# Kernel tuning notes

Hardware: AMD Instinct MI355X
Metric: run time of the kernel (lower is better)

The kernel has to match this reference:

```python
import jax, jax.numpy as jnp
import numpy as np

EPS = 1e-5  # torch LayerNorm default
H = 8       # num_heads


def _ln(x, w, b):
    mu = jnp.mean(x, axis=-1, keepdims=True)
    var = jnp.mean(jnp.square(x - mu), axis=-1, keepdims=True)
    return (x - mu) * jax.lax.rsqrt(var + EPS) * w + b


def setup_inputs() -> dict:
    key = jax.random.key(0)
    ks = jax.random.split(key, 8)
    B, N, C = 4, 2048, 512
    d_ff = 4 * C
    g = lambda k, shape: jax.random.normal(k, shape, jnp.float32) * 0.02
    return {
        "x": jax.random.normal(ks[0], (B, N, C), jnp.float32),
        "e": jax.random.normal(ks[1], (B, N, C), jnp.float32),
        "w_qkv": g(ks[2], (C, 3 * C)),
        "w_s": g(ks[3], (C, C)),
        "w_gate": g(ks[4], (C, C)),
        "w_proj": g(ks[5], (C, C)),
        "b_proj": jnp.zeros((C,), jnp.float32),
        "ln1_w": jnp.ones((C,), jnp.float32), "ln1_b": jnp.zeros((C,), jnp.float32),
        "ln2_w": jnp.ones((C,), jnp.float32), "ln2_b": jnp.zeros((C,), jnp.float32),
        "ln3_w": jnp.ones((C,), jnp.float32), "ln3_b": jnp.zeros((C,), jnp.float32),
        "w_fc1": g(ks[6], (C, d_ff)), "b_fc1": jnp.zeros((d_ff,), jnp.float32),
        "w_fc2": g(ks[7], (d_ff, C)), "b_fc2": jnp.zeros((C,), jnp.float32),
    }


def reference(x, e, w_qkv, w_s, w_gate, w_proj, b_proj,
              ln1_w, ln1_b, ln2_w, ln2_b, ln3_w, ln3_b,
              w_fc1, b_fc1, w_fc2, b_fc2):
    B, N, C = x.shape
    D = C // H
    scale = D ** -0.5  # qk_scale=None -> (dim//num_heads)**-0.5

    # --- attention branch: x + attn(norm1(x), norm2(e)) ---
    xn = _ln(x, ln1_w, ln1_b)
    en = _ln(e, ln2_w, ln2_b)
    qkv = (xn @ w_qkv).reshape(B, N, 3, H, D).transpose(2, 0, 3, 1, 4)  # [3,B,H,N,D]
    q, k, v = qkv[0], qkv[1], qkv[2]
    s = (en @ w_s).reshape(B, N, H, D).transpose(0, 2, 1, 3)            # [B,H,N,D]
    attn = jax.nn.softmax(jnp.einsum('bhnd,bhmd->bhnm', q, k + s) * scale, axis=-1)
    o = jnp.einsum('bhnm,bhmd->bhnd', attn, v).transpose(0, 2, 1, 3).reshape(B, N, C)
    o = (o * (xn @ w_gate)) @ w_proj + b_proj
    x = x + o  # drop_path is identity (drop_prob=0)

    # --- MLP branch: x + mlp(norm3(x)) ---
    xn3 = _ln(x, ln3_w, ln3_b)
    h = jax.nn.gelu(xn3 @ w_fc1 + b_fc1, approximate=False)  # torch nn.GELU = exact erf
    return x + (h @ w_fc2 + b_fc2)
```

## Files before the change

kernel.cpp:

```cpp
#include <hip/hip_runtime.h>

typedef unsigned short u16;
typedef short s16;
typedef u16 u16x4 __attribute__((ext_vector_type(4)));
typedef u16 u16x8 __attribute__((ext_vector_type(8)));
typedef s16 s16x8 __attribute__((ext_vector_type(8)));
typedef float f32x4 __attribute__((ext_vector_type(4)));

__device__ __forceinline__ float b2f(u16 u) {
  union { unsigned int i; float f; } v;
  v.i = ((unsigned int)u) << 16;
  return v.f;
}
__device__ __forceinline__ u16 f2b(float f) {
  union { float f; unsigned int i; } v;
  v.f = f;
  unsigned int r = v.i + 0x7fffu + ((v.i >> 16) & 1u);
  return (u16)(r >> 16);
}

#define MFMA16(a, b, c) __builtin_amdgcn_mfma_f32_16x16x32_bf16(a, b, c, 0, 0, 0)

__device__ __forceinline__ void gld16(const u16* g, u16* l) {
  __builtin_amdgcn_global_load_lds(
      (const __attribute__((address_space(1))) void*)g,
      (__attribute__((address_space(3))) void*)l, 16, 0, 0);
}

__global__ __launch_bounds__(256) void ln12_kernel(
    const float* __restrict__ x, const float* __restrict__ e,
    const float* __restrict__ w1, const float* __restrict__ b1,
    const float* __restrict__ w2, const float* __restrict__ b2,
    u16* __restrict__ xn, u16* __restrict__ en) {
  int bid = blockIdx.x;
  const float *inv, *w, *bb;
  u16* out;
  if (bid < 2048) { inv = x; w = w1; bb = b1; out = xn; }
  else { bid -= 2048; inv = e; w = w2; bb = b2; out = en; }
  const int row = bid * 4 + (threadIdx.x >> 6);
  const int lane = threadIdx.x & 63;
  const float* p = inv + (size_t)row * 512 + lane * 8;
  f32x4 v0 = *(const f32x4*)p;
  f32x4 v1 = *(const f32x4*)(p + 4);
  float xv[8];
#pragma unroll
  for (int i = 0; i < 4; i++) { xv[i] = v0[i]; xv[4 + i] = v1[i]; }
  float s = 0.f;
#pragma unroll
  for (int i = 0; i < 8; i++) s += xv[i];
#pragma unroll
  for (int m = 1; m < 64; m <<= 1) s += __shfl_xor(s, m, 64);
  const float mu = s * (1.0f / 512.0f);
  float vs = 0.f;
#pragma unroll
  for (int i = 0; i < 8; i++) { const float d = xv[i] - mu; vs += d * d; }
#pragma unroll
  for (int m = 1; m < 64; m <<= 1) vs += __shfl_xor(vs, m, 64);
  const float r = rsqrtf(vs * (1.0f / 512.0f) + 1e-5f);
  const f32x4 w0 = *(const f32x4*)(w + lane * 8);
  const f32x4 w1v = *(const f32x4*)(w + lane * 8 + 4);
  const f32x4 bb0 = *(const f32x4*)(bb + lane * 8);
  const f32x4 bb1 = *(const f32x4*)(bb + lane * 8 + 4);
  u16x8 ov;
#pragma unroll
  for (int i = 0; i < 4; i++) {
    ov[i] = f2b((xv[i] - mu) * r * w0[i] + bb0[i]);
    ov[4 + i] = f2b((xv[4 + i] - mu) * r * w1v[i] + bb1[i]);
  }
  *(u16x8*)(out + (size_t)row * 512 + lane * 8) = ov;
}

__global__ __launch_bounds__(256) void ln_kernel(const float* __restrict__ inv,
                                                 const float* __restrict__ w,
                                                 const float* __restrict__ bvec,
                                                 u16* __restrict__ out) {
  const int row = blockIdx.x * 4 + (threadIdx.x >> 6);
  const int lane = threadIdx.x & 63;
  const float* p = inv + (size_t)row * 512 + lane * 8;
  f32x4 v0 = *(const f32x4*)p;
  f32x4 v1 = *(const f32x4*)(p + 4);
  float x[8];
#pragma unroll
  for (int i = 0; i < 4; i++) { x[i] = v0[i]; x[4 + i] = v1[i]; }
  float s = 0.f;
#pragma unroll
  for (int i = 0; i < 8; i++) s += x[i];
#pragma unroll
  for (int m = 1; m < 64; m <<= 1) s += __shfl_xor(s, m, 64);
  const float mu = s * (1.0f / 512.0f);
  float vs = 0.f;
#pragma unroll
  for (int i = 0; i < 8; i++) { const float d = x[i] - mu; vs += d * d; }
#pragma unroll
  for (int m = 1; m < 64; m <<= 1) vs += __shfl_xor(vs, m, 64);
  const float r = rsqrtf(vs * (1.0f / 512.0f) + 1e-5f);
  const f32x4 w0 = *(const f32x4*)(w + lane * 8);
  const f32x4 w1 = *(const f32x4*)(w + lane * 8 + 4);
  const f32x4 b0 = *(const f32x4*)(bvec + lane * 8);
  const f32x4 b1 = *(const f32x4*)(bvec + lane * 8 + 4);
  u16x8 ov;
#pragma unroll
  for (int i = 0; i < 4; i++) {
    ov[i] = f2b((x[i] - mu) * r * w0[i] + b0[i]);
    ov[4 + i] = f2b((x[4 + i] - mu) * r * w1[i] + b1[i]);
  }
  *(u16x8*)(out + (size_t)row * 512 + lane * 8) = ov;
}

__global__ __launch_bounds__(256) void wprep_kernel(
    const float* __restrict__ wq, const float* __restrict__ wsc,
    const float* __restrict__ wg, const float* __restrict__ wp,
    const float* __restrict__ w1, const float* __restrict__ w2,
    u16* __restrict__ wqgT, u16* __restrict__ wsT, u16* __restrict__ wpT,
    u16* __restrict__ wf1T, u16* __restrict__ wf2T) {
  __shared__ float T[64][65];
  int bid = blockIdx.x;
  const float* src; u16* dst; int K, N, ntiles;
  if (bid < 192)      { src = wq;  dst = wqgT;              K = 512;  N = 1536; ntiles = 24; }
  else if (bid < 256) { src = wg;  dst = wqgT + 1536 * 512; K = 512;  N = 512;  ntiles = 8; bid -= 192; }
  else if (bid < 320) { src = wsc; dst = wsT;               K = 512;  N = 512;  ntiles = 8; bid -= 256; }
  else if (bid < 384) { src = wp;  dst = wpT;               K = 512;  N = 512;  ntiles = 8; bid -= 320; }
  else if (bid < 640) { src = w1;  dst = wf1T;              K = 512;  N = 2048; ntiles = 32; bid -= 384; }
  else                { src = w2;  dst = wf2T;              K = 2048; N = 512;  ntiles = 8; bid -= 640; }
  const int n0 = (bid % ntiles) * 64, k0 = (bid / ntiles) * 64;
  const int c = threadIdx.x & 63, r0 = threadIdx.x >> 6;
#pragma unroll
  for (int i = 0; i < 16; i++) {
    const int r = i * 4 + r0;
    T[r][c] = src[(size_t)(k0 + r) * N + n0 + c];
  }
  __syncthreads();
#pragma unroll
  for (int i = 0; i < 16; i++) {
    const int r = i * 4 + r0;
    dst[(size_t)(n0 + r) * K + k0 + c] = f2b(T[c][r]);
  }
}

enum { EPI_NONE = 0, EPI_F32RES = 1, EPI_GELU = 2 };

template<int EPI, int BM>
__global__ __launch_bounds__(256) void mgemm(const u16* __restrict__ A,
                                             const u16* __restrict__ Bt,
                                             int M, int N, int K,
                                             u16* __restrict__ Cb, float* Cf,
                                             const float* __restrict__ bias,
                                             const float* resf) {
  constexpr int NT = (BM == 128) ? 4 : 2;
  constexpr int ACH = BM / 32;
  __shared__ u16 As[BM * 64];
  __shared__ u16 Bs[128 * 64];
  const int tid = threadIdx.x;
  const int wv = tid >> 6, lane = tid & 63;
  const int quad = lane >> 4, l16 = lane & 15;
  const int sw = l16 & 7;
  const int wrow = (BM == 128) ? (wv >> 1) * 64 : 0;
  const int wcol = (BM == 128) ? (wv & 1) * 64 : wv * 32;
  const int m0 = blockIdx.y * BM, n0 = blockIdx.x * 128;
  const int lrow = lane >> 3;
  const int lcs = ((lane & 7) ^ lrow) * 8;
  f32x4 acc[4][NT];
#pragma unroll
  for (int i = 0; i < 4; i++)
#pragma unroll
    for (int j = 0; j < NT; j++) acc[i][j] = (f32x4){0.f, 0.f, 0.f, 0.f};
  for (int k0 = 0; k0 < K; k0 += 64) {
    __syncthreads();
#pragma unroll
    for (int i = 0; i < ACH; i++) {
      const int ch = wv * ACH + i;
      gld16(A + (size_t)(m0 + ch * 8 + lrow) * K + k0 + lcs, &As[ch * 512]);
    }
#pragma unroll
    for (int i = 0; i < 4; i++) {
      const int ch = wv * 4 + i;
      gld16(Bt + (size_t)(n0 + ch * 8 + lrow) * K + k0 + lcs, &Bs[ch * 512]);
    }
    __syncthreads();
#pragma unroll
    for (int ks = 0; ks < 2; ks++) {
      s16x8 af[4], bf[NT];
#pragma unroll
      for (int mt = 0; mt < 4; mt++)
        af[mt] = *(const s16x8*)&As[(wrow + mt * 16 + l16) * 64 +
                                    (((ks * 4 + quad) ^ sw) * 8)];
#pragma unroll
      for (int nt = 0; nt < NT; nt++)
        bf[nt] = *(const s16x8*)&Bs[(wcol + nt * 16 + l16) * 64 +
                                    (((ks * 4 + quad) ^ sw) * 8)];
#pragma unroll
      for (int mt = 0; mt < 4; mt++)
#pragma unroll
        for (int nt = 0; nt < NT; nt++)
          acc[mt][nt] = MFMA16(af[mt], bf[nt], acc[mt][nt]);
    }
  }
#pragma unroll
  for (int nt = 0; nt < NT; nt++) {
    const int n = n0 + wcol + nt * 16 + l16;
    const float bn = (EPI != EPI_NONE) ? bias[n] : 0.f;
#pragma unroll
    for (int mt = 0; mt < 4; mt++) {
#pragma unroll
      for (int r = 0; r < 4; r++) {
        const int m = m0 + wrow + mt * 16 + quad * 4 + r;
        float v = acc[mt][nt][r] + bn;
        if (EPI == EPI_GELU)
          v = 0.5f * v * (1.0f + erff(v * 0.70710678118654752f));
        if (EPI == EPI_F32RES) {
          const size_t idx = (size_t)m * N + n;
          Cf[idx] = v + resf[idx];
        } else {
          Cb[(size_t)m * N + n] = f2b(v);
        }
      }
    }
  }
}

__global__ __launch_bounds__(256) void ksvt_kernel(const u16* __restrict__ qg,
                                                   const u16* __restrict__ sb,
                                                   u16* __restrict__ ksg,
                                                   u16* __restrict__ vtg) {
  __shared__ u16 T[64 * 72];
  const int bh = blockIdx.y;
  const int b = bh >> 3, h = bh & 7;
  const int kk0 = blockIdx.x * 64;
  const size_t rb = (size_t)b * 2048;
  const size_t base = (size_t)bh * 131072;
  const int row = threadIdx.x >> 2, cb = (threadIdx.x & 3) * 16;
  const u16* kp = qg + (rb + kk0 + row) * 2048 + 512 + h * 64 + cb;
  const u16* sp = sb + (rb + kk0 + row) * 512 + h * 64 + cb;
  const u16x8 k0v = *(const u16x8*)kp;
  const u16x8 k1v = *(const u16x8*)(kp + 8);
  const u16x8 s0v = *(const u16x8*)sp;
  const u16x8 s1v = *(const u16x8*)(sp + 8);
  u16x8 o0, o1;
#pragma unroll
  for (int i = 0; i < 8; i++) {
    o0[i] = f2b(b2f(k0v[i]) + b2f(s0v[i]));
    o1[i] = f2b(b2f(k1v[i]) + b2f(s1v[i]));
  }
  *(u16x8*)(ksg + base + (size_t)(kk0 + row) * 64 + cb) = o0;
  *(u16x8*)(ksg + base + (size_t)(kk0 + row) * 64 + cb + 8) = o1;
  const u16x8 v0v = *(const u16x8*)(kp + 512);
  const u16x8 v1v = *(const u16x8*)(kp + 520);
  *(u16x8*)&T[row * 72 + cb] = v0v;
  *(u16x8*)&T[row * 72 + cb + 8] = v1v;
  __syncthreads();
  u16x8 a0, a1;
#pragma unroll
  for (int i = 0; i < 8; i++) {
    a0[i] = T[(cb + i) * 72 + row];
    a1[i] = T[(cb + 8 + i) * 72 + row];
  }
  *(u16x8*)(vtg + base + (size_t)row * 2048 + kk0 + cb) = a0;
  *(u16x8*)(vtg + base + (size_t)row * 2048 + kk0 + cb + 8) = a1;
}

__global__ __launch_bounds__(256) void attn_kernel(const u16* __restrict__ qg,
                                                   const u16* __restrict__ ksg,
                                                   const u16* __restrict__ vtg,
                                                   u16* __restrict__ og) {
  __shared__ u16 KSs[64 * 64];
  __shared__ u16 VTs[64 * 64];
  __shared__ u16 PS[4][16 * 72];
  const int tid = threadIdx.x;
  const int w = tid >> 6, lane = tid & 63;
  const int quad = lane >> 4, l16 = lane & 15;
  const int sw = l16 & 7;
  const int q0 = blockIdx.x * 64;
  const int bh = blockIdx.y;
  const int h = bh & 7;
  const size_t rb = (size_t)(bh >> 3) * 2048;
  const size_t base = (size_t)bh * 131072;
  const int lrow = lane >> 3;
  const int lcs = ((lane & 7) ^ lrow) * 8;

  s16x8 aq[2];
  {
    const u16* qp = qg + (rb + q0 + w * 16 + l16) * 2048 + h * 64 + quad * 8;
#pragma unroll
    for (int ks = 0; ks < 2; ks++) {
      const u16x8 qv = *(const u16x8*)(qp + ks * 32);
      s16x8 t;
#pragma unroll
      for (int i = 0; i < 8; i++) t[i] = (s16)f2b(b2f(qv[i]) * 0.125f);
      aq[ks] = t;
    }
  }
  float m_run = -1e30f, l_run = 0.f;
  f32x4 oacc[4];
#pragma unroll
  for (int nt = 0; nt < 4; nt++) oacc[nt] = (f32x4){0.f, 0.f, 0.f, 0.f};

  for (int kt = 0; kt < 32; kt++) {
    const int kk0 = kt * 64;
    __syncthreads();
#pragma unroll
    for (int i = 0; i < 2; i++) {
      const int ch = w * 2 + i;
      gld16(ksg + base + (size_t)(kk0 + ch * 8 + lrow) * 64 + lcs, &KSs[ch * 512]);
      gld16(vtg + base + (size_t)(ch * 8 + lrow) * 2048 + kk0 + lcs, &VTs[ch * 512]);
    }
    __syncthreads();
    f32x4 sacc[4];
#pragma unroll
    for (int mt = 0; mt < 4; mt++) sacc[mt] = (f32x4){0.f, 0.f, 0.f, 0.f};
#pragma unroll
    for (int ks = 0; ks < 2; ks++) {
#pragma unroll
      for (int mt = 0; mt < 4; mt++) {
        const s16x8 kf = *(const s16x8*)&KSs[(mt * 16 + l16) * 64 +
                                             (((ks * 4 + quad) ^ sw) * 8)];
        sacc[mt] = MFMA16(kf, aq[ks], sacc[mt]);
      }
    }
    float lm = -1e30f;
#pragma unroll
    for (int mt = 0; mt < 4; mt++)
#pragma unroll
      for (int r = 0; r < 4; r++) lm = fmaxf(lm, sacc[mt][r]);
    lm = fmaxf(lm, __shfl_xor(lm, 16, 64));
    lm = fmaxf(lm, __shfl_xor(lm, 32, 64));
    const float mn = fmaxf(m_run, lm);
    const float alpha = __expf(m_run - mn);
    m_run = mn;
    float ls = 0.f;
#pragma unroll
    for (int mt = 0; mt < 4; mt++) {
#pragma unroll
      for (int r = 0; r < 4; r++) {
        const float pv = __expf(sacc[mt][r] - mn);
        sacc[mt][r] = pv;
        ls += pv;
      }
    }
    ls += __shfl_xor(ls, 16, 64);
    ls += __shfl_xor(ls, 32, 64);
    l_run = l_run * alpha + ls;
#pragma unroll
    for (int mt = 0; mt < 4; mt++) {
      u16x4 pk;
#pragma unroll
      for (int r = 0; r < 4; r++) pk[r] = f2b(sacc[mt][r]);
      *(u16x4*)&PS[w][l16 * 72 + mt * 16 + quad * 4] = pk;
    }
#pragma unroll
    for (int r = 0; r < 4; r++) {
      const float af = __shfl(alpha, quad * 4 + r, 64);
#pragma unroll
      for (int nt = 0; nt < 4; nt++) oacc[nt][r] *= af;
    }
#pragma unroll
    for (int ks = 0; ks < 2; ks++) {
      const s16x8 pf = *(const s16x8*)&PS[w][l16 * 72 + ks * 32 + quad * 8];
#pragma unroll
      for (int nt = 0; nt < 4; nt++) {
        const s16x8 vf = *(const s16x8*)&VTs[(nt * 16 + l16) * 64 +
                                             (((ks * 4 + quad) ^ sw) * 8)];
        oacc[nt] = MFMA16(pf, vf, oacc[nt]);
      }
    }
  }
#pragma unroll
  for (int r = 0; r < 4; r++) {
    const float linv = 1.0f / __shfl(l_run, quad * 4 + r, 64);
    const size_t grow = (rb + q0 + w * 16 + quad * 4 + r) * 2048 + 1536 + h * 64;
    const size_t rowb = (rb + q0 + w * 16 + quad * 4 + r) * 512 + h * 64;
#pragma unroll
    for (int nt = 0; nt < 4; nt++) {
      const float g = b2f(qg[grow + nt * 16 + l16]);
      og[rowb + nt * 16 + l16] = f2b(oacc[nt][r] * linv * g);
    }
  }
}

extern "C" void kernel_launch(void* const* d_in, const int* in_sizes, int n_in,
                              void* d_out, int out_size, void* d_ws, size_t ws_size,
                              hipStream_t stream) {
  const float* x      = (const float*)d_in[0];
  const float* e      = (const float*)d_in[1];
  const float* w_qkv  = (const float*)d_in[2];
  const float* w_s    = (const float*)d_in[3];
  const float* w_gate = (const float*)d_in[4];
  const float* w_proj = (const float*)d_in[5];
  const float* b_proj = (const float*)d_in[6];
  const float* ln1w   = (const float*)d_in[7];
  const float* ln1b   = (const float*)d_in[8];
  const float* ln2w   = (const float*)d_in[9];
  const float* ln2b   = (const float*)d_in[10];
  const float* ln3w   = (const float*)d_in[11];
  const float* ln3b   = (const float*)d_in[12];
  const float* w_fc1  = (const float*)d_in[13];
  const float* b_fc1  = (const float*)d_in[14];
  const float* w_fc2  = (const float*)d_in[15];
  const float* b_fc2  = (const float*)d_in[16];
  float* out = (float*)d_out;
  char* ws = (char*)d_ws;

  u16* xn    = (u16*)(ws + 0);
  u16* en    = (u16*)(ws + 8388608);
  u16* qg    = (u16*)(ws + 16777216);
  u16* sbuf  = (u16*)(ws + 50331648);
  u16* obuf  = (u16*)(ws + 58720256);
  u16* wqgT  = (u16*)(ws + 67108864);
  u16* wsT   = (u16*)(ws + 69206016);
  u16* wpT   = (u16*)(ws + 69730304);
  u16* wf1T  = (u16*)(ws + 70254592);
  u16* wf2T  = (u16*)(ws + 72351744);
  u16* vtg   = (u16*)(ws + 74448896);
  u16* ksg   = en;
  u16* hbuf  = qg;
  u16* xn3   = xn;

  dim3 blk(256);
  wprep_kernel<<<896, blk, 0, stream>>>(w_qkv, w_s, w_gate, w_proj, w_fc1, w_fc2,
                                        wqgT, wsT, wpT, wf1T, wf2T);
  ln12_kernel<<<4096, blk, 0, stream>>>(x, e, ln1w, ln1b, ln2w, ln2b, xn, en);
  mgemm<EPI_NONE, 128><<<dim3(16, 64), blk, 0, stream>>>(
      xn, wqgT, 8192, 2048, 512, qg, nullptr, nullptr, nullptr);
  mgemm<EPI_NONE, 64><<<dim3(4, 128), blk, 0, stream>>>(
      en, wsT, 8192, 512, 512, sbuf, nullptr, nullptr, nullptr);
  ksvt_kernel<<<dim3(32, 32), blk, 0, stream>>>(qg, sbuf, ksg, vtg);
  attn_kernel<<<dim3(32, 32), blk, 0, stream>>>(qg, ksg, vtg, obuf);
  mgemm<EPI_F32RES, 64><<<dim3(4, 128), blk, 0, stream>>>(
      obuf, wpT, 8192, 512, 512, nullptr, out, b_proj, x);
  ln_kernel<<<2048, blk, 0, stream>>>(out, ln3w, ln3b, xn3);
  mgemm<EPI_GELU, 128><<<dim3(16, 64), blk, 0, stream>>>(
      xn3, wf1T, 8192, 2048, 512, hbuf, nullptr, b_fc1, nullptr);
  mgemm<EPI_F32RES, 64><<<dim3(4, 128), blk, 0, stream>>>(
      hbuf, wf2T, 8192, 512, 2048, nullptr, out, b_fc2, out);
  (void)in_sizes; (void)n_in; (void)out_size; (void)ws_size;
}
```

Measured before the change: 351.1 us.

## Double query rows per attention block and add BK template to narrow GEMMs

The attention kernel now handles 128 query rows per block, with each wave owning two 16-row groups. Each K/V tile loaded into shared memory is reused across twice as many queries, which halves the grid and the K/V global traffic. Separately, the GEMM gains a BK template parameter, and the narrow-N GEMMs use a 128-wide K step, which halves the number of k-loop iterations and barriers. The trade-offs are higher register pressure in attention, larger LDS footprints, and fewer blocks to cover the GPU.

```diff
diff --git a/kernel.cpp b/kernel.cpp
--- a/kernel.cpp
+++ b/kernel.cpp
@@ -139,7 +139,7 @@
 
 enum { EPI_NONE = 0, EPI_F32RES = 1, EPI_GELU = 2 };
 
-template<int EPI, int BM>
+template<int EPI, int BM, int BK>
 __global__ __launch_bounds__(256) void mgemm(const u16* __restrict__ A,
                                              const u16* __restrict__ Bt,
                                              int M, int N, int K,
@@ -147,9 +147,12 @@
                                              const float* __restrict__ bias,
                                              const float* resf) {
   constexpr int NT = (BM == 128) ? 4 : 2;
-  constexpr int ACH = BM / 32;
-  __shared__ u16 As[BM * 64];
-  __shared__ u16 Bs[128 * 64];
+  constexpr int ACHW = BM * BK / 512 / 4;
+  constexpr int BCHW = 128 * BK / 512 / 4;
+  constexpr int LPR = BK / 8;
+  constexpr int RPC = 512 / BK;
+  __shared__ u16 As[BM * BK];
+  __shared__ u16 Bs[128 * BK];
   const int tid = threadIdx.x;
   const int wv = tid >> 6, lane = tid & 63;
   const int quad = lane >> 4, l16 = lane & 15;
@@ -157,36 +160,38 @@
   const int wrow = (BM == 128) ? (wv >> 1) * 64 : 0;
   const int wcol = (BM == 128) ? (wv & 1) * 64 : wv * 32;
   const int m0 = blockIdx.y * BM, n0 = blockIdx.x * 128;
-  const int lrow = lane >> 3;
-  const int lcs = ((lane & 7) ^ lrow) * 8;
+  const int lrow = lane / LPR;
+  const int inrow = lane % LPR;
   f32x4 acc[4][NT];
 #pragma unroll
   for (int i = 0; i < 4; i++)
 #pragma unroll
     for (int j = 0; j < NT; j++) acc[i][j] = (f32x4){0.f, 0.f, 0.f, 0.f};
-  for (int k0 = 0; k0 < K; k0 += 64) {
+  for (int k0 = 0; k0 < K; k0 += BK) {
     __syncthreads();
 #pragma unroll
-    for (int i = 0; i < ACH; i++) {
-      const int ch = wv * ACH + i;
-      gld16(A + (size_t)(m0 + ch * 8 + lrow) * K + k0 + lcs, &As[ch * 512]);
-    }
-#pragma unroll
-    for (int i = 0; i < 4; i++) {
-      const int ch = wv * 4 + i;
-      gld16(Bt + (size_t)(n0 + ch * 8 + lrow) * K + k0 + lcs, &Bs[ch * 512]);
+    for (int i = 0; i < ACHW; i++) {
+      const int ch = wv * ACHW + i;
+      const int r = ch * RPC + lrow;
+      gld16(A + (size_t)(m0 + r) * K + k0 + ((inrow ^ (r & 7)) * 8), &As[ch * 512]);
+    }
+#pragma unroll
+    for (int i = 0; i < BCHW; i++) {
+      const int ch = wv * BCHW + i;
+      const int r = ch * RPC + lrow;
+      gld16(Bt + (size_t)(n0 + r) * K + k0 + ((inrow ^ (r & 7)) * 8), &Bs[ch * 512]);
     }
     __syncthreads();
 #pragma unroll
-    for (int ks = 0; ks < 2; ks++) {
+    for (int ks = 0; ks < BK / 32; ks++) {
       s16x8 af[4], bf[NT];
 #pragma unroll
       for (int mt = 0; mt < 4; mt++)
-        af[mt] = *(const s16x8*)&As[(wrow + mt * 16 + l16) * 64 +
+        af[mt] = *(const s16x8*)&As[(wrow + mt * 16 + l16) * BK +
                                     (((ks * 4 + quad) ^ sw) * 8)];
 #pragma unroll
       for (int nt = 0; nt < NT; nt++)
-        bf[nt] = *(const s16x8*)&Bs[(wcol + nt * 16 + l16) * 64 +
+        bf[nt] = *(const s16x8*)&Bs[(wcol + nt * 16 + l16) * BK +
                                     (((ks * 4 + quad) ^ sw) * 8)];
 #pragma unroll
       for (int mt = 0; mt < 4; mt++)
@@ -264,12 +269,12 @@
                                                    u16* __restrict__ og) {
   __shared__ u16 KSs[64 * 64];
   __shared__ u16 VTs[64 * 64];
-  __shared__ u16 PS[4][16 * 72];
+  __shared__ u16 PS[4][32 * 72];
   const int tid = threadIdx.x;
   const int w = tid >> 6, lane = tid & 63;
   const int quad = lane >> 4, l16 = lane & 15;
   const int sw = l16 & 7;
-  const int q0 = blockIdx.x * 64;
+  const int q0 = blockIdx.x * 128;
   const int bh = blockIdx.y;
   const int h = bh & 7;
   const size_t rb = (size_t)(bh >> 3) * 2048;
@@ -277,22 +282,25 @@
   const int lrow = lane >> 3;
   const int lcs = ((lane & 7) ^ lrow) * 8;
 
-  s16x8 aq[2];
-  {
-    const u16* qp = qg + (rb + q0 + w * 16 + l16) * 2048 + h * 64 + quad * 8;
+  s16x8 aq[2][2];
+#pragma unroll
+  for (int g = 0; g < 2; g++) {
+    const u16* qp = qg + (rb + q0 + w * 32 + g * 16 + l16) * 2048 + h * 64 + quad * 8;
 #pragma unroll
     for (int ks = 0; ks < 2; ks++) {
       const u16x8 qv = *(const u16x8*)(qp + ks * 32);
       s16x8 t;
 #pragma unroll
       for (int i = 0; i < 8; i++) t[i] = (s16)f2b(b2f(qv[i]) * 0.125f);
-      aq[ks] = t;
-    }
-  }
-  float m_run = -1e30f, l_run = 0.f;
-  f32x4 oacc[4];
-#pragma unroll
-  for (int nt = 0; nt < 4; nt++) oacc[nt] = (f32x4){0.f, 0.f, 0.f, 0.f};
+      aq[g][ks] = t;
+    }
+  }
+  float m_run[2] = {-1e30f, -1e30f}, l_run[2] = {0.f, 0.f};
+  f32x4 oacc[2][4];
+#pragma unroll
+  for (int g = 0; g < 2; g++)
+#pragma unroll
+    for (int nt = 0; nt < 4; nt++) oacc[g][nt] = (f32x4){0.f, 0.f, 0.f, 0.f};
 
   for (int kt = 0; kt < 32; kt++) {
     const int kk0 = kt * 64;
@@ -304,74 +312,91 @@
       gld16(vtg + base + (size_t)(ch * 8 + lrow) * 2048 + kk0 + lcs, &VTs[ch * 512]);
     }
     __syncthreads();
-    f32x4 sacc[4];
-#pragma unroll
-    for (int mt = 0; mt < 4; mt++) sacc[mt] = (f32x4){0.f, 0.f, 0.f, 0.f};
+    f32x4 sacc[2][4];
+#pragma unroll
+    for (int g = 0; g < 2; g++)
+#pragma unroll
+      for (int mt = 0; mt < 4; mt++) sacc[g][mt] = (f32x4){0.f, 0.f, 0.f, 0.f};
 #pragma unroll
     for (int ks = 0; ks < 2; ks++) {
 #pragma unroll
       for (int mt = 0; mt < 4; mt++) {
         const s16x8 kf = *(const s16x8*)&KSs[(mt * 16 + l16) * 64 +
                                              (((ks * 4 + quad) ^ sw) * 8)];
-        sacc[mt] = MFMA16(kf, aq[ks], sacc[mt]);
-      }
-    }
-    float lm = -1e30f;
-#pragma unroll
-    for (int mt = 0; mt < 4; mt++)
-#pragma unroll
-      for (int r = 0; r < 4; r++) lm = fmaxf(lm, sacc[mt][r]);
-    lm = fmaxf(lm, __shfl_xor(lm, 16, 64));
-    lm = fmaxf(lm, __shfl_xor(lm, 32, 64));
-    const float mn = fmaxf(m_run, lm);
-    const float alpha = __expf(m_run - mn);
-    m_run = mn;
-    float ls = 0.f;
-#pragma unroll
-    for (int mt = 0; mt < 4; mt++) {
+#pragma unroll
+        for (int g = 0; g < 2; g++)
+          sacc[g][mt] = MFMA16(kf, aq[g][ks], sacc[g][mt]);
+      }
+    }
+    float alpha[2];
+#pragma unroll
+    for (int g = 0; g < 2; g++) {
+      float lm = -1e30f;
+#pragma unroll
+      for (int mt = 0; mt < 4; mt++)
+#pragma unroll
+        for (int r = 0; r < 4; r++) lm = fmaxf(lm, sacc[g][mt][r]);
+      lm = fmaxf(lm, __shfl_xor(lm, 16, 64));
+      lm = fmaxf(lm, __shfl_xor(lm, 32, 64));
+      const float mn = fmaxf(m_run[g], lm);
+      alpha[g] = __expf(m_run[g] - mn);
+      m_run[g] = mn;
+      float ls = 0.f;
+#pragma unroll
+      for (int mt = 0; mt < 4; mt++) {
+#pragma unroll
+        for (int r = 0; r < 4; r++) {
+          const float pv = __expf(sacc[g][mt][r] - mn);
+          sacc[g][mt][r] = pv;
+          ls += pv;
+        }
+      }
+      ls += __shfl_xor(ls, 16, 64);
+      ls += __shfl_xor(ls, 32, 64);
+      l_run[g] = l_run[g] * alpha[g] + ls;
+#pragma unroll
+      for (int mt = 0; mt < 4; mt++) {
+        u16x4 pk;
+#pragma unroll
+        for (int r = 0; r < 4; r++) pk[r] = f2b(sacc[g][mt][r]);
+        *(u16x4*)&PS[w][(g * 16 + l16) * 72 + mt * 16 + quad * 4] = pk;
+      }
 #pragma unroll
       for (int r = 0; r < 4; r++) {
-        const float pv = __expf(sacc[mt][r] - mn);
-        sacc[mt][r] = pv;
-        ls += pv;
-      }
-    }
-    ls += __shfl_xor(ls, 16, 64);
-    ls += __shfl_xor(ls, 32, 64);
-    l_run = l_run * alpha + ls;
-#pragma unroll
-    for (int mt = 0; mt < 4; mt++) {
-      u16x4 pk;
-#pragma unroll
-      for (int r = 0; r < 4; r++) pk[r] = f2b(sacc[mt][r]);
-      *(u16x4*)&PS[w][l16 * 72 + mt * 16 + quad * 4] = pk;
-    }
-#pragma unroll
-    for (int r = 0; r < 4; r++) {
-      const float af = __shfl(alpha, quad * 4 + r, 64);
-#pragma unroll
-      for (int nt = 0; nt < 4; nt++) oacc[nt][r] *= af;
+        const float af = __shfl(alpha[g], quad * 4 + r, 64);
+#pragma unroll
+        for (int nt = 0; nt < 4; nt++) oacc[g][nt][r] *= af;
+      }
     }
 #pragma unroll
     for (int ks = 0; ks < 2; ks++) {
-      const s16x8 pf = *(const s16x8*)&PS[w][l16 * 72 + ks * 32 + quad * 8];
+      s16x8 pf[2];
+#pragma unroll
+      for (int g = 0; g < 2; g++)
+        pf[g] = *(const s16x8*)&PS[w][(g * 16 + l16) * 72 + ks * 32 + quad * 8];
 #pragma unroll
       for (int nt = 0; nt < 4; nt++) {
         const s16x8 vf = *(const s16x8*)&VTs[(nt * 16 + l16) * 64 +
                                              (((ks * 4 + quad) ^ sw) * 8)];
-        oacc[nt] = MFMA16(pf, vf, oacc[nt]);
-      }
-    }
-  }
-#pragma unroll
-  for (int r = 0; r < 4; r++) {
-    const float linv = 1.0f / __shfl(l_run, quad * 4 + r, 64);
-    const size_t grow = (rb + q0 + w * 16 + quad * 4 + r) * 2048 + 1536 + h * 64;
-    const size_t rowb = (rb + q0 + w * 16 + quad * 4 + r) * 512 + h * 64;
-#pragma unroll
-    for (int nt = 0; nt < 4; nt++) {
-      const float g = b2f(qg[grow + nt * 16 + l16]);
-      og[rowb + nt * 16 + l16] = f2b(oacc[nt][r] * linv * g);
+#pragma unroll
+        for (int g = 0; g < 2; g++)
+          oacc[g][nt] = MFMA16(pf[g], vf, oacc[g][nt]);
+      }
+    }
+  }
+#pragma unroll
+  for (int g = 0; g < 2; g++) {
+#pragma unroll
+    for (int r = 0; r < 4; r++) {
+      const float linv = 1.0f / __shfl(l_run[g], quad * 4 + r, 64);
+      const size_t qrow = rb + q0 + w * 32 + g * 16 + quad * 4 + r;
+      const size_t grow = qrow * 2048 + 1536 + h * 64;
+      const size_t rowb = qrow * 512 + h * 64;
+#pragma unroll
+      for (int nt = 0; nt < 4; nt++) {
+        const float gv = b2f(qg[grow + nt * 16 + l16]);
+        og[rowb + nt * 16 + l16] = f2b(oacc[g][nt][r] * linv * gv);
+      }
     }
   }
 }
@@ -418,18 +443,18 @@
   wprep_kernel<<<896, blk, 0, stream>>>(w_qkv, w_s, w_gate, w_proj, w_fc1, w_fc2,
                                         wqgT, wsT, wpT, wf1T, wf2T);
   ln12_kernel<<<4096, blk, 0, stream>>>(x, e, ln1w, ln1b, ln2w, ln2b, xn, en);
-  mgemm<EPI_NONE, 128><<<dim3(16, 64), blk, 0, stream>>>(
+  mgemm<EPI_NONE, 128, 64><<<dim3(16, 64), blk, 0, stream>>>(
       xn, wqgT, 8192, 2048, 512, qg, nullptr, nullptr, nullptr);
-  mgemm<EPI_NONE, 64><<<dim3(4, 128), blk, 0, stream>>>(
+  mgemm<EPI_NONE, 64, 128><<<dim3(4, 128), blk, 0, stream>>>(
       en, wsT, 8192, 512, 512, sbuf, nullptr, nullptr, nullptr);
   ksvt_kernel<<<dim3(32, 32), blk, 0, stream>>>(qg, sbuf, ksg, vtg);
-  attn_kernel<<<dim3(32, 32), blk, 0, stream>>>(qg, ksg, vtg, obuf);
-  mgemm<EPI_F32RES, 64><<<dim3(4, 128), blk, 0, stream>>>(
+  attn_kernel<<<dim3(16, 32), blk, 0, stream>>>(qg, ksg, vtg, obuf);
+  mgemm<EPI_F32RES, 64, 128><<<dim3(4, 128), blk, 0, stream>>>(
       obuf, wpT, 8192, 512, 512, nullptr, out, b_proj, x);
   ln_kernel<<<2048, blk, 0, stream>>>(out, ln3w, ln3b, xn3);
-  mgemm<EPI_GELU, 128><<<dim3(16, 64), blk, 0, stream>>>(
+  mgemm<EPI_GELU, 128, 64><<<dim3(16, 64), blk, 0, stream>>>(
       xn3, wf1T, 8192, 2048, 512, hbuf, nullptr, b_fc1, nullptr);
-  mgemm<EPI_F32RES, 64><<<dim3(4, 128), blk, 0, stream>>>(
+  mgemm<EPI_F32RES, 64, 128><<<dim3(4, 128), blk, 0, stream>>>(
       hbuf, wf2T, 8192, 512, 2048, nullptr, out, b_fc2, out);
   (void)in_sizes; (void)n_in; (void)out_size; (void)ws_size;
 }
```

After: 356.0 us. About the same (+1.4%).
